# Kernel tuning notes

Measured on AMD Instinct MI355X. Metric: run time of the kernel, lower is better.

Reference implementation:

```python
import jax, jax.numpy as jnp
import numpy as np

EPS = 1e-13


def _masked_softmax(logits, mask_last):
    # logits: [B, Q, K]; mask_last: [B, 1, K] float {0,1}
    # Faithful to torch source: multiply logits by mask (NOT additive -inf),
    # softmax, re-mask, renormalize.
    p = jax.nn.softmax(logits * mask_last, axis=-1) * mask_last
    return p / (jnp.sum(p, axis=-1, keepdims=True) + EPS)


def setup_inputs() -> dict:
    key = jax.random.key(0)
    k1, k2, k3, k4 = jax.random.split(key, 4)
    B, LA, LB, H = 16, 1024, 1024, 512
    premise_batch = jax.random.normal(k1, (B, LA, H), dtype=jnp.float32)
    hypothesis_batch = jax.random.normal(k2, (B, LB, H), dtype=jnp.float32)
    premise_mask = jax.random.randint(k3, (B, LA), 0, 2).astype(jnp.float32)
    hypothesis_mask = jax.random.randint(k4, (B, LB), 0, 2).astype(jnp.float32)
    # avoid fully-masked rows (degenerate)
    premise_mask = premise_mask.at[:, 0].set(1.0)
    hypothesis_mask = hypothesis_mask.at[:, 0].set(1.0)
    return {
        "premise_batch": premise_batch,
        "premise_mask": premise_mask,
        "hypothesis_batch": hypothesis_batch,
        "hypothesis_mask": hypothesis_mask,
    }


def reference(premise_batch, premise_mask, hypothesis_batch, hypothesis_mask):
    # sim[b,i,j] = <a_i, b_j>
    sim = jnp.einsum("bih,bjh->bij", premise_batch, hypothesis_batch)
    prem_hyp_attn = _masked_softmax(sim, hypothesis_mask[:, None, :])           # [B,LA,LB]
    hyp_prem_attn = _masked_softmax(sim.transpose(0, 2, 1), premise_mask[:, None, :])  # [B,LB,LA]
    attended_premises = jnp.einsum("bij,bjh->bih", prem_hyp_attn, hypothesis_batch)
    attended_premises = attended_premises * premise_mask[:, :, None]
    attended_hypotheses = jnp.einsum("bji,bjh->bih", hyp_prem_attn.transpose(0, 2, 1), premise_batch)
    attended_hypotheses = attended_hypotheses * hypothesis_mask[:, :, None]
    return (attended_premises, attended_hypotheses)
```

## Files before the change

kernel.cpp:

```cpp
#include <hip/hip_runtime.h>
#include <math.h>

#define NB   16
#define SLA  1024
#define SLB  1024
#define HH   512

typedef __attribute__((ext_vector_type(4))) float  f32x4;
typedef __attribute__((ext_vector_type(8))) short  s16x8;
typedef __attribute__((ext_vector_type(4))) int    i32x4;

#define QS    (6.5f / 127.f)
#define QINVS (127.f / 6.5f)

__device__ __forceinline__ unsigned short f2bf(float x){
  unsigned u = __float_as_uint(x);
  u += 0x7fffu + ((u >> 16) & 1u);
  return (unsigned short)(u >> 16);
}
__device__ __forceinline__ float bf2f(unsigned short h){
  return __uint_as_float(((unsigned)h) << 16);
}
__device__ __forceinline__ unsigned fkey(float f){
  unsigned u = __float_as_uint(f);
  return ((int)u < 0) ? ~u : (u | 0x80000000u);
}
__device__ __forceinline__ float funkey(unsigned k){
  return __uint_as_float((k & 0x80000000u) ? (k & 0x7fffffffu) : ~k);
}

__device__ __forceinline__ void gl2lds16(const void* g, void* l){
  __builtin_amdgcn_global_load_lds(
      (__attribute__((address_space(1))) unsigned int*)(unsigned long long)(size_t)g,
      (__attribute__((address_space(3))) unsigned int*)(unsigned int)(size_t)l,
      16, 0, 0);
}

__global__ __launch_bounds__(256) void init_kernel(
    unsigned* __restrict__ rowMaxU, unsigned* __restrict__ colMaxU,
    float* __restrict__ rowSum, float* __restrict__ colSum)
{
  const int g = blockIdx.x * 256 + threadIdx.x;
  rowMaxU[g] = 0u; colMaxU[g] = 0u;
  rowSum[g] = 0.f; colSum[g] = 0.f;
}

__global__ __launch_bounds__(256) void scan_kernel(
    const float* __restrict__ pmask, const float* __restrict__ hmask,
    int* __restrict__ pIdx, int* __restrict__ hIdx,
    int* __restrict__ pCnt, int* __restrict__ hCnt,
    int* __restrict__ pPad, int* __restrict__ hPad)
{
  __shared__ int ps[256];
  const int b     = blockIdx.x;
  const int which = blockIdx.y;
  const int t     = threadIdx.x;
  const float* m = (which ? hmask : pmask) + b * 1024;
  int* idx = (which ? hIdx : pIdx) + b * 1024;
  int* cnt = which ? hCnt : pCnt;
  int* pad = which ? hPad : pPad;

  int f[4], s = 0;
  #pragma unroll
  for (int e = 0; e < 4; ++e){
    f[e] = m[t * 4 + e] > 0.5f ? 1 : 0;
    s += f[e];
  }
  ps[t] = s;
  __syncthreads();
  for (int off = 1; off < 256; off <<= 1){
    int v = (t >= off) ? ps[t - off] : 0;
    __syncthreads();
    ps[t] += v;
    __syncthreads();
  }
  int pos = ps[t] - s;
  #pragma unroll
  for (int e = 0; e < 4; ++e){
    if (f[e]) idx[pos++] = t * 4 + e;
  }
  if (t == 0){
    int total = ps[255];
    cnt[b] = total;
    pad[b] = (total + 127) & ~127;
  }
}

__global__ __launch_bounds__(256) void zero_out_kernel(
    const float* __restrict__ pmask, const float* __restrict__ hmask,
    float* __restrict__ out)
{
  const int r = blockIdx.x * 4 + (threadIdx.x >> 6);
  const int side = r >> 14;
  const int b    = (r >> 10) & 15;
  const int row  = r & 1023;
  const float mv = (side ? hmask : pmask)[b * 1024 + row];
  if (mv > 0.5f) return;
  float4 z = {0.f, 0.f, 0.f, 0.f};
  float* p = out + (size_t)side * NB * SLA * HH
                 + ((size_t)b * 1024 + row) * 512 + (threadIdx.x & 63) * 8;
  *(float4*)p = z;
  *(float4*)(p + 4) = z;
}

__global__ __launch_bounds__(256) void cvt_gather_kernel(
    const float* __restrict__ prem, const float* __restrict__ hyp,
    const int* __restrict__ pIdx, const int* __restrict__ hIdx,
    const int* __restrict__ pCnt, const int* __restrict__ hCnt,
    const int* __restrict__ pPad, const int* __restrict__ hPad,
    char* __restrict__ premD1, char* __restrict__ premD0,
    char* __restrict__ hypD1,  char* __restrict__ hypD0,
    unsigned short* __restrict__ PremT, unsigned short* __restrict__ HypT)
{
  __shared__ unsigned short tv[64][72];
  __shared__ int sIdx[64];

  const int tensor = blockIdx.z >> 4;
  const int b  = blockIdx.z & 15;
  const int l0 = blockIdx.y * 64;
  const int h0 = blockIdx.x * 64;
  const int t  = threadIdx.x;

  const int cnt = tensor ? hCnt[b] : pCnt[b];
  const int pad = tensor ? hPad[b] : pPad[b];
  if (l0 >= pad) return;

  const float* X = tensor ? hyp : prem;
  const int* idx = (tensor ? hIdx : pIdx) + b * 1024;
  char* D1 = tensor ? hypD1 : premD1;
  char* D0 = tensor ? hypD0 : premD0;
  unsigned short* XT = tensor ? HypT : PremT;

  if (t < 64){
    int jc = l0 + t;
    sIdx[t] = (jc < cnt) ? idx[jc] : -1;
  }
  __syncthreads();

  #pragma unroll
  for (int it = 0; it < 4; ++it){
    int r = (t >> 4) + it * 16;
    int c = (t & 15) * 4;
    int orig = sIdx[r];
    float4 x = {0.f, 0.f, 0.f, 0.f};
    if (orig >= 0)
      x = *(const float4*)(X + ((size_t)b * 1024 + orig) * HH + h0 + c);
    float xv[4] = {x.x, x.y, x.z, x.w};
    char d1v[4], d0v[4];
    #pragma unroll
    for (int e = 0; e < 4; ++e){
      float xs = xv[e] * QINVS;
      float x1 = rintf(xs);
      x1 = fminf(127.f, fmaxf(-127.f, x1));
      float x0 = rintf((xs - x1) * 256.f);
      x0 = fminf(127.f, fmaxf(-128.f, x0));
      d1v[e] = (char)(int)x1;
      d0v[e] = (char)(int)x0;
      tv[c + e][r] = f2bf(xv[e]);
    }
    size_t go = ((size_t)b * 1024 + l0 + r) * HH + h0 + c;
    *(char4*)(D1 + go) = make_char4(d1v[0], d1v[1], d1v[2], d1v[3]);
    *(char4*)(D0 + go) = make_char4(d0v[0], d0v[1], d0v[2], d0v[3]);
  }
  __syncthreads();
  const int w   = t >> 2;
  const int seg = (t & 3) * 16;
  const uint4* src = (const uint4*)&tv[w][seg];
  uint4* dst = (uint4*)(XT + ((size_t)b * HH + h0 + w) * 1024 + l0 + seg);
  dst[0] = src[0];
  dst[1] = src[1];
}

__global__ __launch_bounds__(256, 3) void sim_gemm_v4_kernel(
    const char* __restrict__ premD1, const char* __restrict__ premD0,
    const char* __restrict__ hypD1,  const char* __restrict__ hypD0,
    const int* __restrict__ pCnt, const int* __restrict__ hCnt,
    const int* __restrict__ pPad, const int* __restrict__ hPad,
    float* __restrict__ sim,
    unsigned* __restrict__ rowMaxU, unsigned* __restrict__ colMaxU)
{
  __shared__ char sA1[128 * 64];
  __shared__ char sA0[128 * 64];
  __shared__ char sB1[64 * 64];
  __shared__ char sB0[64 * 64];

  const int b  = blockIdx.z;
  const int i0 = blockIdx.y * 128;
  const int j0 = blockIdx.x * 64;
  const int t  = threadIdx.x;

  const int pc = pCnt[b], hc = hCnt[b];
  if (i0 >= pPad[b] || j0 >= hPad[b]) return;

  const char* A1 = premD1 + ((size_t)b * 1024 + i0) * HH;
  const char* A0 = premD0 + ((size_t)b * 1024 + i0) * HH;
  const char* B1 = hypD1  + ((size_t)b * 1024 + j0) * HH;
  const char* B0 = hypD0  + ((size_t)b * 1024 + j0) * HH;

  const int sr = t >> 2;
  const int gc = ((t & 3) ^ (sr & 3)) * 16;
  const int lco = (t & 3) * 16;

  const int lane = t & 63;
  const int wr = (t >> 7) & 1;
  const int wc = (t >> 6) & 1;
  const int q  = lane >> 4;
  const int ln = lane & 15;
  const int fo = (q ^ (ln & 3)) * 16;

  i32x4 acc1[4][2], accc[4][2];
  #pragma unroll
  for (int mt = 0; mt < 4; ++mt)
    #pragma unroll
    for (int nt = 0; nt < 2; ++nt){
      acc1[mt][nt] = (i32x4){0, 0, 0, 0};
      accc[mt][nt] = (i32x4){0, 0, 0, 0};
    }

  for (int k0 = 0; k0 < HH; k0 += 64){
    __syncthreads();
    {
      const size_t goA = (size_t)sr * HH + k0 + gc;
      gl2lds16(A1 + goA, &sA1[sr * 64 + lco]);
      gl2lds16(A0 + goA, &sA0[sr * 64 + lco]);
      const size_t goA2 = (size_t)(64 + sr) * HH + k0 + gc;
      gl2lds16(A1 + goA2, &sA1[(64 + sr) * 64 + lco]);
      gl2lds16(A0 + goA2, &sA0[(64 + sr) * 64 + lco]);
      gl2lds16(B1 + goA, &sB1[sr * 64 + lco]);
      gl2lds16(B0 + goA, &sB0[sr * 64 + lco]);
    }
    __syncthreads();

    i32x4 af[4], bf1[2], bf0[2];
    #pragma unroll
    for (int mt = 0; mt < 4; ++mt)
      af[mt] = *(const i32x4*)&sA1[(wr * 64 + mt * 16 + ln) * 64 + fo];
    #pragma unroll
    for (int nt = 0; nt < 2; ++nt)
      bf1[nt] = *(const i32x4*)&sB1[(wc * 32 + nt * 16 + ln) * 64 + fo];
    #pragma unroll
    for (int mt = 0; mt < 4; ++mt)
      #pragma unroll
      for (int nt = 0; nt < 2; ++nt)
        acc1[mt][nt] = __builtin_amdgcn_mfma_i32_16x16x64_i8(af[mt], bf1[nt], acc1[mt][nt], 0, 0, 0);
    #pragma unroll
    for (int nt = 0; nt < 2; ++nt)
      bf0[nt] = *(const i32x4*)&sB0[(wc * 32 + nt * 16 + ln) * 64 + fo];
    #pragma unroll
    for (int mt = 0; mt < 4; ++mt)
      #pragma unroll
      for (int nt = 0; nt < 2; ++nt)
        accc[mt][nt] = __builtin_amdgcn_mfma_i32_16x16x64_i8(af[mt], bf0[nt], accc[mt][nt], 0, 0, 0);
    #pragma unroll
    for (int mt = 0; mt < 4; ++mt)
      af[mt] = *(const i32x4*)&sA0[(wr * 64 + mt * 16 + ln) * 64 + fo];
    #pragma unroll
    for (int mt = 0; mt < 4; ++mt)
      #pragma unroll
      for (int nt = 0; nt < 2; ++nt)
        accc[mt][nt] = __builtin_amdgcn_mfma_i32_16x16x64_i8(af[mt], bf1[nt], accc[mt][nt], 0, 0, 0);
  }

  const float S2 = QS * QS;
  float* simb = sim + ((size_t)b * SLA + i0) * SLB + j0;

  float rmx[16];
  #pragma unroll
  for (int e = 0; e < 16; ++e) rmx[e] = -1e30f;
  float cmx[2];
  cmx[0] = -1e30f; cmx[1] = -1e30f;

  #pragma unroll
  for (int mt = 0; mt < 4; ++mt){
    #pragma unroll
    for (int nt = 0; nt < 2; ++nt){
      int col = wc * 32 + nt * 16 + ln;
      bool colv = (j0 + col) < hc;
      #pragma unroll
      for (int rr = 0; rr < 4; ++rr){
        int row = wr * 64 + mt * 16 + q * 4 + rr;
        float f = S2 * ((float)acc1[mt][nt][rr] + (float)accc[mt][nt][rr] * 0.00390625f);
        simb[(size_t)row * SLB + col] = f;
        rmx[mt * 4 + rr] = fmaxf(rmx[mt * 4 + rr], colv ? f : -1e30f);
        cmx[nt] = fmaxf(cmx[nt], (i0 + row) < pc ? f : -1e30f);
      }
    }
  }

  #pragma unroll
  for (int e = 0; e < 16; ++e){
    float v = rmx[e];
    v = fmaxf(v, __shfl_xor(v, 1));
    v = fmaxf(v, __shfl_xor(v, 2));
    v = fmaxf(v, __shfl_xor(v, 4));
    v = fmaxf(v, __shfl_xor(v, 8));
    if (ln == 0){
      int row = wr * 64 + (e >> 2) * 16 + q * 4 + (e & 3);
      if (i0 + row < pc)
        atomicMax(rowMaxU + b * 1024 + i0 + row, fkey(v));
    }
  }
  #pragma unroll
  for (int nt = 0; nt < 2; ++nt){
    float v = cmx[nt];
    v = fmaxf(v, __shfl_xor(v, 16));
    v = fmaxf(v, __shfl_xor(v, 32));
    if (q == 0){
      int col = wc * 32 + nt * 16 + ln;
      if (j0 + col < hc)
        atomicMax(colMaxU + b * 1024 + j0 + col, fkey(v));
    }
  }
}

__global__ __launch_bounds__(256) void inv_kernel(float* __restrict__ rowS,
                                                  float* __restrict__ colS)
{
  const int g = blockIdx.x * 256 + threadIdx.x;
  if (g < 16384)      rowS[g] = 1.f / rowS[g];
  else                colS[g - 16384] = 1.f / colS[g - 16384];
}

__global__ __launch_bounds__(256) void build_p_v4_kernel(
    const float* __restrict__ sim,
    const unsigned* __restrict__ rowMaxU, const unsigned* __restrict__ colMaxU,
    const int* __restrict__ pCnt, const int* __restrict__ hCnt,
    const int* __restrict__ pPad, const int* __restrict__ hPad,
    unsigned short* __restrict__ Pprem, unsigned short* __restrict__ Phyp,
    float* __restrict__ rowSumAcc, float* __restrict__ colSumAcc)
{
  __shared__ unsigned short tp[64][72];
  __shared__ float sRM[64], sCM[64];

  const int b  = blockIdx.z;
  const int i0 = blockIdx.y * 64;
  const int j0 = blockIdx.x * 64;
  const int t  = threadIdx.x;

  const int pc = pCnt[b], hc = hCnt[b];
  if (i0 >= pPad[b] || j0 >= hPad[b]) return;

  {
    int which = t >> 6, idx = t & 63;
    if (which == 0) sRM[idx] = funkey(rowMaxU[b * 1024 + i0 + idx]);
    if (which == 1) sCM[idx] = funkey(colMaxU[b * 1024 + j0 + idx]);
  }
  __syncthreads();

  const float* sb = sim + (size_t)b * SLA * SLB;
  #pragma unroll
  for (int it = 0; it < 4; ++it){
    int r = (t >> 4) + it * 16;
    int c = (t & 15) * 4;
    float4 s = *(const float4*)(sb + (size_t)(i0 + r) * SLB + j0 + c);
    float rm = sRM[r];
    bool vi = (i0 + r) < pc;
    float p0 = (vi && (j0 + c + 0) < hc) ? __expf(s.x - rm) : 0.f;
    float p1 = (vi && (j0 + c + 1) < hc) ? __expf(s.y - rm) : 0.f;
    float p2 = (vi && (j0 + c + 2) < hc) ? __expf(s.z - rm) : 0.f;
    float p3 = (vi && (j0 + c + 3) < hc) ? __expf(s.w - rm) : 0.f;
    uint2 pk;
    pk.x = (unsigned)f2bf(p0) | ((unsigned)f2bf(p1) << 16);
    pk.y = (unsigned)f2bf(p2) | ((unsigned)f2bf(p3) << 16);
    *(uint2*)(Pprem + ((size_t)b * 1024 + i0 + r) * 1024 + j0 + c) = pk;

    float rs = p0 + p1 + p2 + p3;
    rs += __shfl_xor(rs, 1);
    rs += __shfl_xor(rs, 2);
    rs += __shfl_xor(rs, 4);
    rs += __shfl_xor(rs, 8);
    if ((t & 15) == 0 && vi)
      atomicAdd(rowSumAcc + b * 1024 + i0 + r, rs);

    tp[c + 0][r] = f2bf((vi && (j0 + c + 0) < hc) ? __expf(s.x - sCM[c+0]) : 0.f);
    tp[c + 1][r] = f2bf((vi && (j0 + c + 1) < hc) ? __expf(s.y - sCM[c+1]) : 0.f);
    tp[c + 2][r] = f2bf((vi && (j0 + c + 2) < hc) ? __expf(s.z - sCM[c+2]) : 0.f);
    tp[c + 3][r] = f2bf((vi && (j0 + c + 3) < hc) ? __expf(s.w - sCM[c+3]) : 0.f);
  }
  __syncthreads();
  const int w   = t >> 2;
  const int seg = (t & 3) * 16;
  const uint4* src = (const uint4*)&tp[w][seg];
  uint4 u0 = src[0], u1 = src[1];
  uint4* dst = (uint4*)(Phyp + ((size_t)b * 1024 + j0 + w) * 1024 + i0 + seg);
  dst[0] = u0;
  dst[1] = u1;

  const unsigned short* us0 = (const unsigned short*)&u0;
  const unsigned short* us1 = (const unsigned short*)&u1;
  float cs = 0.f;
  #pragma unroll
  for (int e = 0; e < 8; ++e) cs += bf2f(us0[e]);
  #pragma unroll
  for (int e = 0; e < 8; ++e) cs += bf2f(us1[e]);
  cs += __shfl_xor(cs, 1);
  cs += __shfl_xor(cs, 2);
  if ((t & 3) == 0 && (j0 + w) < hc)
    atomicAdd(colSumAcc + b * 1024 + j0 + w, cs);
}

__global__ __launch_bounds__(256) void av_v4_kernel(
    const unsigned short* __restrict__ Pprem, const unsigned short* __restrict__ Phyp,
    const unsigned short* __restrict__ HypT,  const unsigned short* __restrict__ PremT,
    const float* __restrict__ rowInv, const float* __restrict__ colInv,
    const int* __restrict__ pIdx, const int* __restrict__ hIdx,
    const int* __restrict__ pCnt, const int* __restrict__ hCnt,
    const int* __restrict__ pPad, const int* __restrict__ hPad,
    float* __restrict__ out)
{
  __shared__ unsigned short sA[128 * 64];
  __shared__ unsigned short sB[128 * 64];
  __shared__ float sInv[128];
  __shared__ int sIdx[128];

  const int side = blockIdx.z >> 4;
  const int b    = blockIdx.z & 15;
  const int m0   = blockIdx.y * 128;
  const int n0   = blockIdx.x * 128;
  const int t    = threadIdx.x;

  const int cnt  = side ? hCnt[b] : pCnt[b];
  const int mpad = side ? hPad[b] : pPad[b];
  const int kpad = side ? pPad[b] : hPad[b];
  if (m0 >= mpad) return;

  const unsigned short* A  = (side ? Phyp : Pprem) + (size_t)b * 1024 * 1024;
  const unsigned short* Bt = (side ? PremT : HypT) + (size_t)b * 512 * 1024;
  const float* inv = (side ? colInv : rowInv) + b * 1024;
  const int* idx   = (side ? hIdx : pIdx) + b * 1024;
  float* o = out + (size_t)side * NB * SLA * HH + (size_t)b * 1024 * 512;

  if (t < 128){
    sInv[t] = inv[m0 + t];
    sIdx[t] = idx[m0 + t];
  }

  const int wv = t >> 6;
  const int L  = t & 63;
  const int lr = L >> 3;
  const int sw = L & 7;
  const int gkc = (sw ^ lr) * 8;

  const int lane = t & 63;
  const int wr = (t >> 7) & 1;
  const int wc = (t >> 6) & 1;
  const int q  = lane >> 4;
  const int ln = lane & 15;
  const int fsw = ln & 7;

  f32x4 acc[4][4];
  #pragma unroll
  for (int mt = 0; mt < 4; ++mt)
    #pragma unroll
    for (int nt = 0; nt < 4; ++nt)
      acc[mt][nt] = (f32x4){0.f, 0.f, 0.f, 0.f};

  for (int k0 = 0; k0 < kpad; k0 += 64){
    __syncthreads();
    #pragma unroll
    for (int s = 0; s < 4; ++s){
      int row = wv * 32 + s * 8 + lr;
      gl2lds16(A  + (size_t)(m0 + row) * 1024 + k0 + gkc, &sA[row * 64 + sw * 8]);
      gl2lds16(Bt + (size_t)(n0 + row) * 1024 + k0 + gkc, &sB[row * 64 + sw * 8]);
    }
    __syncthreads();

    #pragma unroll
    for (int h = 0; h < 2; ++h){
      s16x8 af[4], bfr[4];
      #pragma unroll
      for (int mt = 0; mt < 4; ++mt){
        int r = wr * 64 + mt * 16 + ln;
        af[mt] = *(const s16x8*)&sA[r * 64 + (((h << 2) + q) ^ fsw) * 8];
      }
      #pragma unroll
      for (int nt = 0; nt < 4; ++nt){
        int r = wc * 64 + nt * 16 + ln;
        bfr[nt] = *(const s16x8*)&sB[r * 64 + (((h << 2) + q) ^ fsw) * 8];
      }
      #pragma unroll
      for (int mt = 0; mt < 4; ++mt)
        #pragma unroll
        for (int nt = 0; nt < 4; ++nt)
          acc[mt][nt] = __builtin_amdgcn_mfma_f32_16x16x32_bf16(af[mt], bfr[nt], acc[mt][nt], 0, 0, 0);
    }
  }

  #pragma unroll
  for (int mt = 0; mt < 4; ++mt)
    #pragma unroll
    for (int nt = 0; nt < 4; ++nt){
      int col = n0 + wc * 64 + nt * 16 + ln;
      #pragma unroll
      for (int rr = 0; rr < 4; ++rr){
        int rowL = wr * 64 + mt * 16 + q * 4 + rr;
        if (m0 + rowL < cnt)
          o[(size_t)sIdx[rowL] * 512 + col] = acc[mt][nt][rr] * sInv[rowL];
      }
    }
}

extern "C" void kernel_launch(void* const* d_in, const int* in_sizes, int n_in,
                              void* d_out, int out_size, void* d_ws, size_t ws_size,
                              hipStream_t stream)
{
  const float* prem  = (const float*)d_in[0];
  const float* pmask = (const float*)d_in[1];
  const float* hyp   = (const float*)d_in[2];
  const float* hmask = (const float*)d_in[3];
  float* out = (float*)d_out;

  char* ws = (char*)d_ws;
  float*    sim     = (float*)(ws);
  unsigned* rowMaxU = (unsigned*)(ws + 67108864);
  float*    rowInv  = (float*)(ws + 67108864 + 1 * 65536);
  unsigned* colMaxU = (unsigned*)(ws + 67108864 + 2 * 65536);
  float*    colInv  = (float*)(ws + 67108864 + 3 * 65536);
  int* pIdx = (int*)(ws + 67108864 + 4 * 65536);
  int* hIdx = (int*)(ws + 67108864 + 5 * 65536);
  int* pCnt = (int*)(ws + 67108864 + 6 * 65536);
  int* hCnt = (int*)(ws + 67108864 + 6 * 65536 + 256);
  int* pPad = (int*)(ws + 67108864 + 6 * 65536 + 512);
  int* hPad = (int*)(ws + 67108864 + 6 * 65536 + 768);
  const size_t base2 = 67108864 + 4 * 65536 + 1048576;
  char* premD1 = (char*)(ws + base2);
  char* premD0 = (char*)(ws + base2 + 8388608);
  char* hypD1  = (char*)(ws + base2 + 16777216);
  char* hypD0  = (char*)(ws + base2 + 25165824);
  unsigned short* PremT = (unsigned short*)(ws + base2 + 33554432);
  unsigned short* HypT  = (unsigned short*)(ws + base2 + 50331648);
  unsigned short* Pprem = (unsigned short*)(ws + base2);
  unsigned short* Phyp  = (unsigned short*)(ws + base2 + 67108864);
  const size_t need = base2 + 100663296;
  if (ws_size < need) return;

  init_kernel<<<dim3(64), 256, 0, stream>>>(rowMaxU, colMaxU, rowInv, colInv);
  scan_kernel<<<dim3(16, 2), 256, 0, stream>>>(pmask, hmask, pIdx, hIdx,
                                               pCnt, hCnt, pPad, hPad);
  zero_out_kernel<<<dim3(8192), 256, 0, stream>>>(pmask, hmask, out);
  cvt_gather_kernel<<<dim3(8, 16, 32), 256, 0, stream>>>(
      prem, hyp, pIdx, hIdx, pCnt, hCnt, pPad, hPad,
      premD1, premD0, hypD1, hypD0, PremT, HypT);
  sim_gemm_v4_kernel<<<dim3(16, 8, NB), 256, 0, stream>>>(
      premD1, premD0, hypD1, hypD0, pCnt, hCnt, pPad, hPad,
      sim, rowMaxU, colMaxU);
  build_p_v4_kernel<<<dim3(16, 16, NB), 256, 0, stream>>>(
      sim, rowMaxU, colMaxU, pCnt, hCnt, pPad, hPad,
      Pprem, Phyp, rowInv, colInv);
  inv_kernel<<<dim3(128), 256, 0, stream>>>(rowInv, colInv);
  av_v4_kernel<<<dim3(4, 8, 32), 256, 0, stream>>>(
      Pprem, Phyp, HypT, PremT, rowInv, colInv,
      pIdx, hIdx, pCnt, hCnt, pPad, hPad, out);
}
```

Baseline: 220.3 us.

## Store sim in fp16 and fuse row-softmax exp into the AV GEMM

The similarity matrix is now written as fp16 instead of fp32, which halves its write and read traffic. The premise-side softmax is no longer materialized: the AV kernel reads fp16 sim, applies exp(s - rowmax) on the fly, writes bf16 into LDS, and accumulates row sums locally. The init and inv kernels are folded into scan and AV to cut launches. In exchange, fp16 storage loses precision on sim, and side 0 of the AV kernel does exp work on the load path, which may stall the MFMA pipeline since its loads are no longer asynchronous.

```diff
diff --git a/kernel.cpp b/kernel.cpp
--- a/kernel.cpp
+++ b/kernel.cpp
@@ -1,4 +1,5 @@
 #include <hip/hip_runtime.h>
+#include <hip/hip_fp16.h>
 #include <math.h>
 
 #define NB   16
@@ -20,6 +21,9 @@
 }
 __device__ __forceinline__ float bf2f(unsigned short h){
   return __uint_as_float(((unsigned)h) << 16);
+}
+__device__ __forceinline__ float h2f(unsigned short h){
+  return __half2float(__ushort_as_half(h));
 }
 __device__ __forceinline__ unsigned fkey(float f){
   unsigned u = __float_as_uint(f);
@@ -36,20 +40,13 @@
       16, 0, 0);
 }
 
-__global__ __launch_bounds__(256) void init_kernel(
-    unsigned* __restrict__ rowMaxU, unsigned* __restrict__ colMaxU,
-    float* __restrict__ rowSum, float* __restrict__ colSum)
-{
-  const int g = blockIdx.x * 256 + threadIdx.x;
-  rowMaxU[g] = 0u; colMaxU[g] = 0u;
-  rowSum[g] = 0.f; colSum[g] = 0.f;
-}
-
 __global__ __launch_bounds__(256) void scan_kernel(
     const float* __restrict__ pmask, const float* __restrict__ hmask,
     int* __restrict__ pIdx, int* __restrict__ hIdx,
     int* __restrict__ pCnt, int* __restrict__ hCnt,
-    int* __restrict__ pPad, int* __restrict__ hPad)
+    int* __restrict__ pPad, int* __restrict__ hPad,
+    unsigned* __restrict__ rowMaxU, unsigned* __restrict__ colMaxU,
+    float* __restrict__ colSum)
 {
   __shared__ int ps[256];
   const int b     = blockIdx.x;
@@ -59,6 +56,17 @@
   int* idx = (which ? hIdx : pIdx) + b * 1024;
   int* cnt = which ? hCnt : pCnt;
   int* pad = which ? hPad : pPad;
+
+  #pragma unroll
+  for (int v = 0; v < 4; ++v){
+    int g = b * 1024 + t + v * 256;
+    if (which == 0){
+      rowMaxU[g] = 0u;
+    } else {
+      colMaxU[g] = 0u;
+      colSum[g]  = 0.f;
+    }
+  }
 
   int f[4], s = 0;
   #pragma unroll
@@ -171,12 +179,12 @@
   dst[1] = src[1];
 }
 
-__global__ __launch_bounds__(256, 3) void sim_gemm_v4_kernel(
+__global__ __launch_bounds__(256, 3) void sim_gemm_v5_kernel(
     const char* __restrict__ premD1, const char* __restrict__ premD0,
     const char* __restrict__ hypD1,  const char* __restrict__ hypD0,
     const int* __restrict__ pCnt, const int* __restrict__ hCnt,
     const int* __restrict__ pPad, const int* __restrict__ hPad,
-    float* __restrict__ sim,
+    unsigned short* __restrict__ simH,
     unsigned* __restrict__ rowMaxU, unsigned* __restrict__ colMaxU)
 {
   __shared__ char sA1[128 * 64];
@@ -262,7 +270,7 @@
   }
 
   const float S2 = QS * QS;
-  float* simb = sim + ((size_t)b * SLA + i0) * SLB + j0;
+  unsigned short* simb = simH + ((size_t)b * SLA + i0) * SLB + j0;
 
   float rmx[16];
   #pragma unroll
@@ -280,7 +288,7 @@
       for (int rr = 0; rr < 4; ++rr){
         int row = wr * 64 + mt * 16 + q * 4 + rr;
         float f = S2 * ((float)acc1[mt][nt][rr] + (float)accc[mt][nt][rr] * 0.00390625f);
-        simb[(size_t)row * SLB + col] = f;
+        simb[(size_t)row * SLB + col] = __half_as_ushort(__float2half(f));
         rmx[mt * 4 + rr] = fmaxf(rmx[mt * 4 + rr], colv ? f : -1e30f);
         cmx[nt] = fmaxf(cmx[nt], (i0 + row) < pc ? f : -1e30f);
       }
@@ -313,24 +321,15 @@
   }
 }
 
-__global__ __launch_bounds__(256) void inv_kernel(float* __restrict__ rowS,
-                                                  float* __restrict__ colS)
-{
-  const int g = blockIdx.x * 256 + threadIdx.x;
-  if (g < 16384)      rowS[g] = 1.f / rowS[g];
-  else                colS[g - 16384] = 1.f / colS[g - 16384];
-}
-
-__global__ __launch_bounds__(256) void build_p_v4_kernel(
-    const float* __restrict__ sim,
-    const unsigned* __restrict__ rowMaxU, const unsigned* __restrict__ colMaxU,
+__global__ __launch_bounds__(256) void build_pt_kernel(
+    const unsigned short* __restrict__ simH,
+    const unsigned* __restrict__ colMaxU,
     const int* __restrict__ pCnt, const int* __restrict__ hCnt,
     const int* __restrict__ pPad, const int* __restrict__ hPad,
-    unsigned short* __restrict__ Pprem, unsigned short* __restrict__ Phyp,
-    float* __restrict__ rowSumAcc, float* __restrict__ colSumAcc)
+    unsigned short* __restrict__ PhypT, float* __restrict__ colSum)
 {
   __shared__ unsigned short tp[64][72];
-  __shared__ float sRM[64], sCM[64];
+  __shared__ float sCM[64];
 
   const int b  = blockIdx.z;
   const int i0 = blockIdx.y * 64;
@@ -340,49 +339,31 @@
   const int pc = pCnt[b], hc = hCnt[b];
   if (i0 >= pPad[b] || j0 >= hPad[b]) return;
 
-  {
-    int which = t >> 6, idx = t & 63;
-    if (which == 0) sRM[idx] = funkey(rowMaxU[b * 1024 + i0 + idx]);
-    if (which == 1) sCM[idx] = funkey(colMaxU[b * 1024 + j0 + idx]);
-  }
+  if (t < 64) sCM[t] = funkey(colMaxU[b * 1024 + j0 + t]);
   __syncthreads();
 
-  const float* sb = sim + (size_t)b * SLA * SLB;
+  const unsigned short* sb = simH + (size_t)b * SLA * SLB;
   #pragma unroll
   for (int it = 0; it < 4; ++it){
     int r = (t >> 4) + it * 16;
     int c = (t & 15) * 4;
-    float4 s = *(const float4*)(sb + (size_t)(i0 + r) * SLB + j0 + c);
-    float rm = sRM[r];
+    uint2 u = *(const uint2*)(sb + (size_t)(i0 + r) * SLB + j0 + c);
+    float s0 = h2f((unsigned short)(u.x & 0xffff));
+    float s1 = h2f((unsigned short)(u.x >> 16));
+    float s2 = h2f((unsigned short)(u.y & 0xffff));
+    float s3 = h2f((unsigned short)(u.y >> 16));
     bool vi = (i0 + r) < pc;
-    float p0 = (vi && (j0 + c + 0) < hc) ? __expf(s.x - rm) : 0.f;
-    float p1 = (vi && (j0 + c + 1) < hc) ? __expf(s.y - rm) : 0.f;
-    float p2 = (vi && (j0 + c + 2) < hc) ? __expf(s.z - rm) : 0.f;
-    float p3 = (vi && (j0 + c + 3) < hc) ? __expf(s.w - rm) : 0.f;
-    uint2 pk;
-    pk.x = (unsigned)f2bf(p0) | ((unsigned)f2bf(p1) << 16);
-    pk.y = (unsigned)f2bf(p2) | ((unsigned)f2bf(p3) << 16);
-    *(uint2*)(Pprem + ((size_t)b * 1024 + i0 + r) * 1024 + j0 + c) = pk;
-
-    float rs = p0 + p1 + p2 + p3;
-    rs += __shfl_xor(rs, 1);
-    rs += __shfl_xor(rs, 2);
-    rs += __shfl_xor(rs, 4);
-    rs += __shfl_xor(rs, 8);
-    if ((t & 15) == 0 && vi)
-      atomicAdd(rowSumAcc + b * 1024 + i0 + r, rs);
-
-    tp[c + 0][r] = f2bf((vi && (j0 + c + 0) < hc) ? __expf(s.x - sCM[c+0]) : 0.f);
-    tp[c + 1][r] = f2bf((vi && (j0 + c + 1) < hc) ? __expf(s.y - sCM[c+1]) : 0.f);
-    tp[c + 2][r] = f2bf((vi && (j0 + c + 2) < hc) ? __expf(s.z - sCM[c+2]) : 0.f);
-    tp[c + 3][r] = f2bf((vi && (j0 + c + 3) < hc) ? __expf(s.w - sCM[c+3]) : 0.f);
+    tp[c + 0][r] = f2bf((vi && (j0 + c + 0) < hc) ? __expf(s0 - sCM[c+0]) : 0.f);
+    tp[c + 1][r] = f2bf((vi && (j0 + c + 1) < hc) ? __expf(s1 - sCM[c+1]) : 0.f);
+    tp[c + 2][r] = f2bf((vi && (j0 + c + 2) < hc) ? __expf(s2 - sCM[c+2]) : 0.f);
+    tp[c + 3][r] = f2bf((vi && (j0 + c + 3) < hc) ? __expf(s3 - sCM[c+3]) : 0.f);
   }
   __syncthreads();
   const int w   = t >> 2;
   const int seg = (t & 3) * 16;
   const uint4* src = (const uint4*)&tp[w][seg];
   uint4 u0 = src[0], u1 = src[1];
-  uint4* dst = (uint4*)(Phyp + ((size_t)b * 1024 + j0 + w) * 1024 + i0 + seg);
+  uint4* dst = (uint4*)(PhypT + ((size_t)b * 1024 + j0 + w) * 1024 + i0 + seg);
   dst[0] = u0;
   dst[1] = u1;
 
@@ -396,13 +377,14 @@
   cs += __shfl_xor(cs, 1);
   cs += __shfl_xor(cs, 2);
   if ((t & 3) == 0 && (j0 + w) < hc)
-    atomicAdd(colSumAcc + b * 1024 + j0 + w, cs);
-}
-
-__global__ __launch_bounds__(256) void av_v4_kernel(
-    const unsigned short* __restrict__ Pprem, const unsigned short* __restrict__ Phyp,
-    const unsigned short* __restrict__ HypT,  const unsigned short* __restrict__ PremT,
-    const float* __restrict__ rowInv, const float* __restrict__ colInv,
+    atomicAdd(colSum + b * 1024 + j0 + w, cs);
+}
+
+__global__ __launch_bounds__(256, 4) void av2_kernel(
+    const unsigned short* __restrict__ simH,
+    const unsigned short* __restrict__ PhypT,
+    const unsigned short* __restrict__ HypT, const unsigned short* __restrict__ PremT,
+    const unsigned* __restrict__ rowMaxU, const float* __restrict__ colSum,
     const int* __restrict__ pIdx, const int* __restrict__ hIdx,
     const int* __restrict__ pCnt, const int* __restrict__ hCnt,
     const int* __restrict__ pPad, const int* __restrict__ hPad,
@@ -410,8 +392,9 @@
 {
   __shared__ unsigned short sA[128 * 64];
   __shared__ unsigned short sB[128 * 64];
-  __shared__ float sInv[128];
-  __shared__ int sIdx[128];
+  __shared__ float sRM[128];
+  __shared__ float sScale[128];
+  __shared__ int   sIdx[128];
 
   const int side = blockIdx.z >> 4;
   const int b    = blockIdx.z & 15;
@@ -420,19 +403,21 @@
   const int t    = threadIdx.x;
 
   const int cnt  = side ? hCnt[b] : pCnt[b];
+  const int hc   = hCnt[b];
   const int mpad = side ? hPad[b] : pPad[b];
   const int kpad = side ? pPad[b] : hPad[b];
   if (m0 >= mpad) return;
 
-  const unsigned short* A  = (side ? Phyp : Pprem) + (size_t)b * 1024 * 1024;
-  const unsigned short* Bt = (side ? PremT : HypT) + (size_t)b * 512 * 1024;
-  const float* inv = (side ? colInv : rowInv) + b * 1024;
-  const int* idx   = (side ? hIdx : pIdx) + b * 1024;
+  const int* idx = (side ? hIdx : pIdx) + b * 1024;
   float* o = out + (size_t)side * NB * SLA * HH + (size_t)b * 1024 * 512;
 
   if (t < 128){
-    sInv[t] = inv[m0 + t];
     sIdx[t] = idx[m0 + t];
+    if (side){
+      sScale[t] = 1.f / colSum[b * 1024 + m0 + t];
+    } else {
+      sRM[t] = funkey(rowMaxU[b * 1024 + m0 + t]);
+    }
   }
 
   const int wv = t >> 6;
@@ -440,6 +425,9 @@
   const int lr = L >> 3;
   const int sw = L & 7;
   const int gkc = (sw ^ lr) * 8;
+
+  const int ar  = t >> 1;
+  const int akh = (t & 1) * 32;
 
   const int lane = t & 63;
   const int wr = (t >> 7) & 1;
@@ -448,6 +436,12 @@
   const int ln = lane & 15;
   const int fsw = ln & 7;
 
+  const unsigned short* simb  = simH  + (size_t)b * 1024 * 1024;
+  const unsigned short* Ahyp  = PhypT + (size_t)b * 1024 * 1024;
+  const unsigned short* Bt    = (side ? PremT : HypT) + (size_t)b * 512 * 1024;
+
+  float rs = 0.f;
+
   f32x4 acc[4][4];
   #pragma unroll
   for (int mt = 0; mt < 4; ++mt)
@@ -457,11 +451,46 @@
 
   for (int k0 = 0; k0 < kpad; k0 += 64){
     __syncthreads();
-    #pragma unroll
-    for (int s = 0; s < 4; ++s){
-      int row = wv * 32 + s * 8 + lr;
-      gl2lds16(A  + (size_t)(m0 + row) * 1024 + k0 + gkc, &sA[row * 64 + sw * 8]);
-      gl2lds16(Bt + (size_t)(n0 + row) * 1024 + k0 + gkc, &sB[row * 64 + sw * 8]);
+    if (side == 0){
+      #pragma unroll
+      for (int s = 0; s < 4; ++s){
+        int row = wv * 32 + s * 8 + lr;
+        gl2lds16(Bt + (size_t)(n0 + row) * 1024 + k0 + gkc, &sB[row * 64 + sw * 8]);
+      }
+      const unsigned short* sp = simb + (size_t)(m0 + ar) * 1024 + k0 + akh;
+      float rm = sRM[ar];
+      #pragma unroll
+      for (int cc = 0; cc < 4; ++cc){
+        uint4 u = *(const uint4*)(sp + cc * 8);
+        unsigned uw[4] = {u.x, u.y, u.z, u.w};
+        int kb = k0 + akh + cc * 8;
+        unsigned short pb[8];
+        #pragma unroll
+        for (int d = 0; d < 4; ++d){
+          float v0 = h2f((unsigned short)(uw[d] & 0xffff));
+          float v1 = h2f((unsigned short)(uw[d] >> 16));
+          float p0 = (kb + d * 2 + 0) < hc ? __expf(v0 - rm) : 0.f;
+          float p1 = (kb + d * 2 + 1) < hc ? __expf(v1 - rm) : 0.f;
+          rs += p0 + p1;
+          pb[d * 2]     = f2bf(p0);
+          pb[d * 2 + 1] = f2bf(p1);
+        }
+        uint4 w;
+        w.x = (unsigned)pb[0] | ((unsigned)pb[1] << 16);
+        w.y = (unsigned)pb[2] | ((unsigned)pb[3] << 16);
+        w.z = (unsigned)pb[4] | ((unsigned)pb[5] << 16);
+        w.w = (unsigned)pb[6] | ((unsigned)pb[7] << 16);
+        int c   = (t & 1) * 4 + cc;
+        int pos = c ^ (ar & 7);
+        *(uint4*)&sA[ar * 64 + pos * 8] = w;
+      }
+    } else {
+      #pragma unroll
+      for (int s = 0; s < 4; ++s){
+        int row = wv * 32 + s * 8 + lr;
+        gl2lds16(Ahyp + (size_t)(m0 + row) * 1024 + k0 + gkc, &sA[row * 64 + sw * 8]);
+        gl2lds16(Bt   + (size_t)(n0 + row) * 1024 + k0 + gkc, &sB[row * 64 + sw * 8]);
+      }
     }
     __syncthreads();
 
@@ -486,6 +515,13 @@
     }
   }
 
+  if (side == 0){
+    rs += __shfl_xor(rs, 1);
+    __syncthreads();
+    if ((t & 1) == 0) sScale[ar] = 1.f / rs;
+    __syncthreads();
+  }
+
   #pragma unroll
   for (int mt = 0; mt < 4; ++mt)
     #pragma unroll
@@ -495,7 +531,7 @@
       for (int rr = 0; rr < 4; ++rr){
         int rowL = wr * 64 + mt * 16 + q * 4 + rr;
         if (m0 + rowL < cnt)
-          o[(size_t)sIdx[rowL] * 512 + col] = acc[mt][nt][rr] * sInv[rowL];
+          o[(size_t)sIdx[rowL] * 512 + col] = acc[mt][nt][rr] * sScale[rowL];
       }
     }
 }
@@ -511,11 +547,10 @@
   float* out = (float*)d_out;
 
   char* ws = (char*)d_ws;
-  float*    sim     = (float*)(ws);
+  unsigned short* simH = (unsigned short*)(ws);
   unsigned* rowMaxU = (unsigned*)(ws + 67108864);
-  float*    rowInv  = (float*)(ws + 67108864 + 1 * 65536);
   unsigned* colMaxU = (unsigned*)(ws + 67108864 + 2 * 65536);
-  float*    colInv  = (float*)(ws + 67108864 + 3 * 65536);
+  float*    colSum  = (float*)(ws + 67108864 + 3 * 65536);
   int* pIdx = (int*)(ws + 67108864 + 4 * 65536);
   int* hIdx = (int*)(ws + 67108864 + 5 * 65536);
   int* pCnt = (int*)(ws + 67108864 + 6 * 65536);
@@ -529,26 +564,23 @@
   char* hypD0  = (char*)(ws + base2 + 25165824);
   unsigned short* PremT = (unsigned short*)(ws + base2 + 33554432);
   unsigned short* HypT  = (unsigned short*)(ws + base2 + 50331648);
-  unsigned short* Pprem = (unsigned short*)(ws + base2);
-  unsigned short* Phyp  = (unsigned short*)(ws + base2 + 67108864);
+  unsigned short* PhypT = (unsigned short*)(ws + base2);
   const size_t need = base2 + 100663296;
   if (ws_size < need) return;
 
-  init_kernel<<<dim3(64), 256, 0, stream>>>(rowMaxU, colMaxU, rowInv, colInv);
   scan_kernel<<<dim3(16, 2), 256, 0, stream>>>(pmask, hmask, pIdx, hIdx,
-                                               pCnt, hCnt, pPad, hPad);
+                                               pCnt, hCnt, pPad, hPad,
+                                               rowMaxU, colMaxU, colSum);
   zero_out_kernel<<<dim3(8192), 256, 0, stream>>>(pmask, hmask, out);
   cvt_gather_kernel<<<dim3(8, 16, 32), 256, 0, stream>>>(
       prem, hyp, pIdx, hIdx, pCnt, hCnt, pPad, hPad,
       premD1, premD0, hypD1, hypD0, PremT, HypT);
-  sim_gemm_v4_kernel<<<dim3(16, 8, NB), 256, 0, stream>>>(
+  sim_gemm_v5_kernel<<<dim3(16, 8, NB), 256, 0, stream>>>(
       premD1, premD0, hypD1, hypD0, pCnt, hCnt, pPad, hPad,
-      sim, rowMaxU, colMaxU);
-  build_p_v4_kernel<<<dim3(16, 16, NB), 256, 0, stream>>>(
-      sim, rowMaxU, colMaxU, pCnt, hCnt, pPad, hPad,
-      Pprem, Phyp, rowInv, colInv);
-  inv_kernel<<<dim3(128), 256, 0, stream>>>(rowInv, colInv);
-  av_v4_kernel<<<dim3(4, 8, 32), 256, 0, stream>>>(
-      Pprem, Phyp, HypT, PremT, rowInv, colInv,
+      simH, rowMaxU, colMaxU);
+  build_pt_kernel<<<dim3(16, 16, NB), 256, 0, stream>>>(
+      simH, colMaxU, pCnt, hCnt, pPad, hPad, PhypT, colSum);
+  av2_kernel<<<dim3(4, 8, 32), 256, 0, stream>>>(
+      simH, PhypT, HypT, PremT, rowMaxU, colSum,
       pIdx, hIdx, pCnt, hCnt, pPad, hPad, out);
 }
```

Measured after the change: 209.3 us. 5.0% less time.
